# Kernel tuning notes

Hardware: AMD Instinct MI355X
Metric: run time of the kernel (lower is better)

## Reference

```python
import jax, jax.numpy as jnp
import numpy as np

NEG_SLOPE = 0.2  # PyG GATConv default negative_slope


def _gat_layer(x, src, dst, N, W, a_src, a_dst, b):
    """One PyG-style GATConv (eval mode, add_self_loops already applied).
    W: [F_in, H*D], a_src/a_dst: [H, D], b: [H*D]. Returns [N, H*D] (concat)."""
    H, D = a_src.shape
    h = (x @ W).reshape(N, H, D)                      # [N,H,D]
    al_s = (h * a_src).sum(-1)                        # [N,H]
    al_d = (h * a_dst).sum(-1)                        # [N,H]
    e = jax.nn.leaky_relu(al_s[src] + al_d[dst], NEG_SLOPE)   # [E,H]
    # softmax over incoming edges of each destination node
    m = jax.lax.stop_gradient(jax.ops.segment_max(e, dst, num_segments=N))
    ex = jnp.exp(e - m[dst])
    s = jax.ops.segment_sum(ex, dst, num_segments=N)  # [N,H]
    alpha = ex / s[dst]                               # [E,H]
    msg = h[src] * alpha[:, :, None]                  # [E,H,D]
    out = jax.ops.segment_sum(msg, dst, num_segments=N)
    return out.reshape(N, H * D) + b


def setup_inputs() -> dict:
    key = jax.random.key(0)
    ks = jax.random.split(key, 16)
    N, E, F_in, HID, HEADS, C = 50000, 1600000, 128, 8, 8, 16
    x = jax.random.normal(ks[0], (N, F_in), dtype=jnp.float32)
    edge_index = jax.random.randint(ks[1], (2, E), 0, N, dtype=jnp.int64)

    def glorot(k, shape):
        fan = shape[0] + shape[-1]
        return jax.random.uniform(k, shape, jnp.float32, -1.0, 1.0) * np.sqrt(6.0 / fan)

    HD = HID * HEADS  # 64
    return {
        "x": x, "edge_index": edge_index,
        "W1": glorot(ks[2], (F_in, HD)), "a1s": glorot(ks[3], (HEADS, HID)),
        "a1d": glorot(ks[4], (HEADS, HID)), "b1": jnp.zeros((HD,), jnp.float32),
        "W2": glorot(ks[5], (HD, HD)), "a2s": glorot(ks[6], (HEADS, HID)),
        "a2d": glorot(ks[7], (HEADS, HID)), "b2": jnp.zeros((HD,), jnp.float32),
        "W3": glorot(ks[8], (HD, HD)), "a3s": glorot(ks[9], (HEADS, HID)),
        "a3d": glorot(ks[10], (HEADS, HID)), "b3": jnp.zeros((HD,), jnp.float32),
        "W4": glorot(ks[11], (HD, C)), "a4s": glorot(ks[12], (1, C)),
        "a4d": glorot(ks[13], (1, C)), "b4": jnp.zeros((C,), jnp.float32),
    }


def reference(x, edge_index, W1, a1s, a1d, b1, W2, a2s, a2d, b2,
              W3, a3s, a3d, b3, W4, a4s, a4d, b4):
    N = x.shape[0]
    loops = jnp.arange(N, dtype=edge_index.dtype)  # PyG add_self_loops=True
    src = jnp.concatenate([edge_index[0], loops])
    dst = jnp.concatenate([edge_index[1], loops])
    h = jax.nn.relu(_gat_layer(x, src, dst, N, W1, a1s, a1d, b1))
    h = jax.nn.relu(_gat_layer(h, src, dst, N, W2, a2s, a2d, b2))
    h = jax.nn.relu(_gat_layer(h, src, dst, N, W3, a3s, a3d, b3))
    return _gat_layer(h, src, dst, N, W4, a4s, a4d, b4)  # [N, num_classes]
```

## Files before the change

### kernel.cpp

```cpp
#include <hip/hip_runtime.h>
#include <hip/hip_bf16.h>
#include <math.h>

#define NEG_SLOPE 0.2f
#define LOGIT_SHIFT 8.0f

static inline int cdiv(int a, int b) { return (a + b - 1) / b; }

#define BCAP 12288
#define PT_THREADS 512
#define PT_EPT 16
#define PT_CHUNK (PT_THREADS * PT_EPT)

__global__ __launch_bounds__(PT_THREADS)
void partition_kernel(const int* __restrict__ src, const int* __restrict__ dst,
                      unsigned* __restrict__ gcursor, unsigned* __restrict__ slab,
                      int E, int ET, int NBK) {
    __shared__ int hist[256];
    __shared__ int lbase[256];
    __shared__ int lcur[256];
    __shared__ int gbase[256];
    __shared__ unsigned stage[PT_CHUNK];
    __shared__ unsigned char binof[PT_CHUNK];

    int base = blockIdx.x * PT_CHUNK;
    int cnt = min(PT_CHUNK, ET - base);

    unsigned vals[PT_EPT];
    short bins[PT_EPT];

    for (int i = threadIdx.x; i < 256; i += PT_THREADS) hist[i] = 0;
    __syncthreads();

#pragma unroll
    for (int i = 0; i < PT_EPT; ++i) {
        int e = base + threadIdx.x + i * PT_THREADS;
        bins[i] = -1;
        if (e < ET) {
            int s = (e < E) ? src[e] : (e - E);
            int d = (e < E) ? dst[e] : (e - E);
            int b = d >> 8;
            vals[i] = ((unsigned)s << 8) | (unsigned)(d & 255);
            bins[i] = (short)b;
            atomicAdd(&hist[b], 1);
        }
    }
    __syncthreads();
    if (threadIdx.x < 256) lbase[threadIdx.x] = hist[threadIdx.x];
    __syncthreads();
    for (int off = 1; off < 256; off <<= 1) {
        int t = 0;
        if (threadIdx.x < 256 && threadIdx.x >= off) t = lbase[threadIdx.x - off];
        __syncthreads();
        if (threadIdx.x < 256) lbase[threadIdx.x] += t;
        __syncthreads();
    }
    if (threadIdx.x < 256) {
        lbase[threadIdx.x] -= hist[threadIdx.x];
        lcur[threadIdx.x] = lbase[threadIdx.x];
        gbase[threadIdx.x] = ((int)threadIdx.x < NBK && hist[threadIdx.x] > 0)
            ? (int)atomicAdd(&gcursor[threadIdx.x], (unsigned)hist[threadIdx.x]) : 0;
    }
    __syncthreads();
#pragma unroll
    for (int i = 0; i < PT_EPT; ++i) {
        if (bins[i] >= 0) {
            int p = atomicAdd(&lcur[bins[i]], 1);
            stage[p] = vals[i];
            binof[p] = (unsigned char)bins[i];
        }
    }
    __syncthreads();
    for (int j = threadIdx.x; j < cnt; j += PT_THREADS) {
        int b = binof[j];
        int idx = gbase[b] + (j - lbase[b]);
        if (idx < BCAP) slab[(size_t)b * BCAP + idx] = stage[j];
    }
}

__global__ __launch_bounds__(512)
void finalize_kernel(const unsigned* __restrict__ gcursor, unsigned* __restrict__ slab,
                     int* __restrict__ offs, int* __restrict__ deg, int N) {
    __shared__ int lhist[256];
    __shared__ int loff[256];
    __shared__ int lcur[256];
    __shared__ unsigned stage[BCAP];
    int b = blockIdx.x;
    int cnt = min((int)gcursor[b], BCAP);
    int d0 = b << 8;
    int nd = min(256, N - d0);
    size_t sb = (size_t)b * BCAP;

    for (int i = threadIdx.x; i < 256; i += 512) lhist[i] = 0;
    __syncthreads();
    for (int i = threadIdx.x; i < cnt; i += 512)
        atomicAdd(&lhist[slab[sb + i] & 255u], 1);
    __syncthreads();
    if (threadIdx.x < 256) loff[threadIdx.x] = lhist[threadIdx.x];
    __syncthreads();
    for (int off = 1; off < 256; off <<= 1) {
        int t = 0;
        if (threadIdx.x < 256 && threadIdx.x >= off) t = loff[threadIdx.x - off];
        __syncthreads();
        if (threadIdx.x < 256) loff[threadIdx.x] += t;
        __syncthreads();
    }
    if (threadIdx.x < 256) {
        loff[threadIdx.x] -= lhist[threadIdx.x];
        lcur[threadIdx.x] = loff[threadIdx.x];
        if ((int)threadIdx.x < nd) {
            offs[d0 + threadIdx.x] = (int)sb + loff[threadIdx.x];
            deg[d0 + threadIdx.x] = lhist[threadIdx.x];
        }
    }
    __syncthreads();
    for (int i = threadIdx.x; i < cnt; i += 512) {
        unsigned v = slab[sb + i];
        int p = atomicAdd(&lcur[v & 255u], 1);
        stage[p] = v >> 8;
    }
    __syncthreads();
    for (int i = threadIdx.x; i < cnt; i += 512)
        slab[sb + i] = stage[i];
}

template <int CIN, int COUT, int H, bool BF16OUT>
__global__ void gemm_logits_kernel(const float* __restrict__ in, const float* __restrict__ W,
                                   const float* __restrict__ a_s, const float* __restrict__ a_d,
                                   void* __restrict__ outv, float* __restrict__ als,
                                   float* __restrict__ ald, int N) {
    constexpr int D = COUT / H;
    constexpr int TPN = COUT / 4;
    constexpr int NPB = 256 / TPN;
    __shared__ float xs[NPB * CIN];
    __shared__ float lsum[2][NPB][H];
    int n0 = blockIdx.x * NPB;
    for (int i = threadIdx.x * 4; i < NPB * CIN; i += 256 * 4) {
        int n = n0 + i / CIN;
        float4 v = make_float4(0.f, 0.f, 0.f, 0.f);
        if (n < N) v = *(const float4*)&in[(size_t)n0 * CIN + i];
        *(float4*)&xs[i] = v;
    }
    for (int i = threadIdx.x; i < 2 * NPB * H; i += 256) ((float*)lsum)[i] = 0.f;
    __syncthreads();
    int tn = threadIdx.x / TPN;
    int tc = (threadIdx.x % TPN) * 4;
    int n = n0 + tn;
    if (n < N) {
        const float* xr = xs + tn * CIN;
        float4 a = make_float4(0.f, 0.f, 0.f, 0.f);
#pragma unroll 8
        for (int k = 0; k < CIN; ++k) {
            float xv = xr[k];
            float4 wv = *(const float4*)&W[k * COUT + tc];
            a.x = fmaf(xv, wv.x, a.x);
            a.y = fmaf(xv, wv.y, a.y);
            a.z = fmaf(xv, wv.z, a.z);
            a.w = fmaf(xv, wv.w, a.w);
        }
        if (BF16OUT) {
            __hip_bfloat16* ob = (__hip_bfloat16*)outv;
            ushort4 u;
            u.x = __hip_bfloat16_raw(__float2bfloat16(a.x)).x;
            u.y = __hip_bfloat16_raw(__float2bfloat16(a.y)).x;
            u.z = __hip_bfloat16_raw(__float2bfloat16(a.z)).x;
            u.w = __hip_bfloat16_raw(__float2bfloat16(a.w)).x;
            *(ushort4*)&ob[(size_t)n * COUT + tc] = u;
        } else {
            float* of = (float*)outv;
            *(float4*)&of[(size_t)n * COUT + tc] = a;
        }
        int h = tc / D;
        int dd = tc % D;
        const float* asr = a_s + h * D + dd;
        const float* adr = a_d + h * D + dd;
        float p1 = a.x * asr[0] + a.y * asr[1] + a.z * asr[2] + a.w * asr[3];
        float p2 = a.x * adr[0] + a.y * adr[1] + a.z * adr[2] + a.w * adr[3];
        atomicAdd(&lsum[0][tn][h], p1);
        atomicAdd(&lsum[1][tn][h], p2);
    }
    __syncthreads();
    for (int i = threadIdx.x; i < NPB * H; i += 256) {
        int tn2 = i / H, h2 = i % H;
        int n2 = n0 + tn2;
        if (n2 < N) {
            als[n2 * H + h2] = lsum[0][tn2][h2];
            ald[n2 * H + h2] = lsum[1][tn2][h2];
        }
    }
}

__device__ __forceinline__ float lrelu(float x) {
    return (x > 0.f) ? x : NEG_SLOPE * x;
}
__device__ __forceinline__ float edge_w(float logit) {
    return __expf(lrelu(logit) - LOGIT_SHIFT);
}

template <bool RELU>
__global__ void gat_node8_kernel(const __hip_bfloat16* __restrict__ hfeat,
                                 const float* __restrict__ als, const float* __restrict__ ald,
                                 const int* __restrict__ offs, const int* __restrict__ deg,
                                 const int* __restrict__ csr_src,
                                 const float* __restrict__ bias,
                                 float* __restrict__ out, int N) {
    int lane = threadIdx.x & 63;
    int wid = threadIdx.x >> 6;
    int node = blockIdx.x * (blockDim.x >> 6) + wid;
    if (node >= N) return;
    int row = __builtin_amdgcn_readfirstlane(offs[node]);
    int cnt = __builtin_amdgcn_readfirstlane(deg[node]);

    int hl = lane & 7;
    int el = lane >> 3;
    float xd = ald[node * 8 + hl];

    float s0 = 0.f, s1 = 0.f;
    int k = el;
    for (; k + 8 < cnt; k += 16) {
        int snA = csr_src[row + k];
        int snB = csr_src[row + k + 8];
        s0 += edge_w(als[snA * 8 + hl] + xd);
        s1 += edge_w(als[snB * 8 + hl] + xd);
    }
    if (k < cnt) {
        int sn = csr_src[row + k];
        s0 += edge_w(als[sn * 8 + hl] + xd);
    }
    float sl = s0 + s1;
    sl += __shfl_xor(sl, 8);
    sl += __shfl_xor(sl, 16);
    sl += __shfl_xor(sl, 32);

    int c = lane;
    int h2 = lane >> 3;
    float s2 = __shfl(sl, h2);
    float acc = 0.f;
    int kk = el;
    int kc = (kk < cnt) ? kk : (cnt - 1);
    int sn_l = csr_src[row + kc];
    float w_l = (kk < cnt) ? edge_w(als[sn_l * 8 + hl] + xd) : 0.f;
    for (int kb = 0; kb < cnt; kb += 8) {
        int sn_cur = sn_l;
        float w_cur = w_l;
        int kk2 = kb + 8 + el;
        if (kb + 8 < cnt) {
            int kc2 = (kk2 < cnt) ? kk2 : (cnt - 1);
            sn_l = csr_src[row + kc2];
            w_l = (kk2 < cnt) ? edge_w(als[sn_l * 8 + hl] + xd) : 0.f;
        }
#pragma unroll
        for (int e = 0; e < 8; ++e) {
            int srcl = (e << 3) + h2;
            int sn_e = __shfl(sn_cur, srcl);
            float w_e = __shfl(w_cur, srcl);
            float hv = __bfloat162float(hfeat[(size_t)sn_e * 64 + c]);
            acc = fmaf(w_e, hv, acc);
        }
    }
    float v = acc / s2 + bias[c];
    if (RELU) v = fmaxf(v, 0.f);
    out[(size_t)node * 64 + c] = v;
}

__global__ void gat_node16_kernel(const float* __restrict__ hfeat,
                                  const float* __restrict__ als, const float* __restrict__ ald,
                                  const int* __restrict__ offs, const int* __restrict__ deg,
                                  const int* __restrict__ csr_src,
                                  const float* __restrict__ bias,
                                  float* __restrict__ out, int N) {
    int lane = threadIdx.x & 63;
    int wid = threadIdx.x >> 6;
    int node = blockIdx.x * (blockDim.x >> 6) + wid;
    if (node >= N) return;
    int row = __builtin_amdgcn_readfirstlane(offs[node]);
    int cnt = __builtin_amdgcn_readfirstlane(deg[node]);
    float xd = ald[node];

    float s0 = 0.f, s1 = 0.f;
    int k = lane;
    for (; k + 64 < cnt; k += 128) {
        int snA = csr_src[row + k];
        int snB = csr_src[row + k + 64];
        s0 += edge_w(als[snA] + xd);
        s1 += edge_w(als[snB] + xd);
    }
    if (k < cnt) {
        int sn = csr_src[row + k];
        s0 += edge_w(als[sn] + xd);
    }
    float sl = s0 + s1;
#pragma unroll
    for (int off = 1; off < 64; off <<= 1) sl += __shfl_xor(sl, off);

    int c = lane & 15;
    int g = lane >> 4;
    float a0 = 0.f, a1 = 0.f, a2 = 0.f, a3 = 0.f;
    k = g;
    for (; k + 12 < cnt; k += 16) {
        int sn0 = csr_src[row + k];
        int sn1 = csr_src[row + k + 4];
        int sn2 = csr_src[row + k + 8];
        int sn3 = csr_src[row + k + 12];
        float w0 = edge_w(als[sn0] + xd);
        float w1 = edge_w(als[sn1] + xd);
        float w2 = edge_w(als[sn2] + xd);
        float w3 = edge_w(als[sn3] + xd);
        a0 = fmaf(w0, hfeat[(size_t)sn0 * 16 + c], a0);
        a1 = fmaf(w1, hfeat[(size_t)sn1 * 16 + c], a1);
        a2 = fmaf(w2, hfeat[(size_t)sn2 * 16 + c], a2);
        a3 = fmaf(w3, hfeat[(size_t)sn3 * 16 + c], a3);
    }
    for (; k < cnt; k += 4) {
        int sn = csr_src[row + k];
        a0 = fmaf(edge_w(als[sn] + xd), hfeat[(size_t)sn * 16 + c], a0);
    }
    float acc = (a0 + a1) + (a2 + a3);
    acc += __shfl_xor(acc, 16);
    acc += __shfl_xor(acc, 32);
    if (lane < 16) {
        out[(size_t)node * 16 + c] = acc / sl + bias[c];
    }
}


extern "C" void kernel_launch(void* const* d_in, const int* in_sizes, int n_in,
                              void* d_out, int out_size, void* d_ws, size_t ws_size,
                              hipStream_t stream) {
    const float* x   = (const float*)d_in[0];
    const int*   ei  = (const int*)d_in[1];
    const float* W1  = (const float*)d_in[2];
    const float* a1s = (const float*)d_in[3];
    const float* a1d = (const float*)d_in[4];
    const float* b1  = (const float*)d_in[5];
    const float* W2  = (const float*)d_in[6];
    const float* a2s = (const float*)d_in[7];
    const float* a2d = (const float*)d_in[8];
    const float* b2  = (const float*)d_in[9];
    const float* W3  = (const float*)d_in[10];
    const float* a3s = (const float*)d_in[11];
    const float* a3d = (const float*)d_in[12];
    const float* b3  = (const float*)d_in[13];
    const float* W4  = (const float*)d_in[14];
    const float* a4s = (const float*)d_in[15];
    const float* a4d = (const float*)d_in[16];
    const float* b4  = (const float*)d_in[17];

    const int N = in_sizes[0] / 128;
    const int E = in_sizes[1] / 2;
    const int ET = E + N;
    const int* src = ei;
    const int* dst = ei + E;
    const int NBK = (N + 255) >> 8;

    float* hb    = (float*)d_ws;
    float* bufA  = hb + (size_t)N * 64;
    float* als   = bufA + (size_t)N * 64;
    float* ald   = als + (size_t)N * 8;
    int* offs    = (int*)(ald + (size_t)N * 8);
    int* deg     = offs + N;
    unsigned* gcursor = (unsigned*)(deg + N);
    unsigned* slab = gcursor + 256;
    float* out = (float*)d_out;

    __hip_bfloat16* hb16 = (__hip_bfloat16*)hb;

    const int TB = 256;
    const int NODE_BLOCKS = cdiv(N, 4);

    hipMemsetAsync(gcursor, 0, 256 * 4, stream);
    partition_kernel<<<cdiv(ET, PT_CHUNK), PT_THREADS, 0, stream>>>(src, dst, gcursor, slab, E, ET, NBK);
    finalize_kernel<<<NBK, 512, 0, stream>>>(gcursor, slab, offs, deg, N);
    const int* csr_src = (const int*)slab;

    gemm_logits_kernel<128, 64, 8, true><<<cdiv(N, 16), TB, 0, stream>>>(x, W1, a1s, a1d, hb16, als, ald, N);
    gat_node8_kernel<true><<<NODE_BLOCKS, TB, 0, stream>>>(hb16, als, ald, offs, deg, csr_src, b1, bufA, N);

    gemm_logits_kernel<64, 64, 8, true><<<cdiv(N, 16), TB, 0, stream>>>(bufA, W2, a2s, a2d, hb16, als, ald, N);
    gat_node8_kernel<true><<<NODE_BLOCKS, TB, 0, stream>>>(hb16, als, ald, offs, deg, csr_src, b2, bufA, N);

    gemm_logits_kernel<64, 64, 8, true><<<cdiv(N, 16), TB, 0, stream>>>(bufA, W3, a3s, a3d, hb16, als, ald, N);
    gat_node8_kernel<true><<<NODE_BLOCKS, TB, 0, stream>>>(hb16, als, ald, offs, deg, csr_src, b3, bufA, N);

    gemm_logits_kernel<64, 16, 1, false><<<cdiv(N, 64), TB, 0, stream>>>(bufA, W4, a4s, a4d, hb, als, ald, N);
    gat_node16_kernel<<<NODE_BLOCKS, TB, 0, stream>>>(hb, als, ald, offs, deg, csr_src, b4, out, N);
}
```

Measured before the change: 491.2 us.

## Fuse softmax denominator into single-pass aggregation with vectorized per-edge feature loads

Both GAT node kernels drop the separate pass that computed the softmax denominator. Each lane now owns one edge and one head/column chunk, loads 8 bf16 (or 4 fp32) features as a single vector, and accumulates the weighted sum and the denominator together. Partial results are then reduced with cross-lane shuffles. This removes the duplicate csr_src/als gathers and the per-edge shuffles of the old code, at the cost of more registers and a longer butterfly reduction at the end.

```diff
diff --git a/kernel.cpp b/kernel.cpp
--- a/kernel.cpp
+++ b/kernel.cpp
@@ -211,56 +211,64 @@
     int row = __builtin_amdgcn_readfirstlane(offs[node]);
     int cnt = __builtin_amdgcn_readfirstlane(deg[node]);
 
-    int hl = lane & 7;
     int el = lane >> 3;
-    float xd = ald[node * 8 + hl];
-
-    float s0 = 0.f, s1 = 0.f;
-    int k = el;
-    for (; k + 8 < cnt; k += 16) {
-        int snA = csr_src[row + k];
-        int snB = csr_src[row + k + 8];
-        s0 += edge_w(als[snA * 8 + hl] + xd);
-        s1 += edge_w(als[snB * 8 + hl] + xd);
-    }
-    if (k < cnt) {
-        int sn = csr_src[row + k];
-        s0 += edge_w(als[sn * 8 + hl] + xd);
-    }
-    float sl = s0 + s1;
-    sl += __shfl_xor(sl, 8);
-    sl += __shfl_xor(sl, 16);
-    sl += __shfl_xor(sl, 32);
-
-    int c = lane;
-    int h2 = lane >> 3;
-    float s2 = __shfl(sl, h2);
-    float acc = 0.f;
+    int cb = lane & 7;
+    float xd = ald[node * 8 + cb];
+
+    float s = 0.f;
+    float acc[8];
+#pragma unroll
+    for (int j = 0; j < 8; ++j) acc[j] = 0.f;
+
     int kk = el;
     int kc = (kk < cnt) ? kk : (cnt - 1);
-    int sn_l = csr_src[row + kc];
-    float w_l = (kk < cnt) ? edge_w(als[sn_l * 8 + hl] + xd) : 0.f;
+    int sn_c = csr_src[row + kc];
+    float al_c = als[sn_c * 8 + cb];
+    uint4 hv_c = *(const uint4*)(hfeat + (size_t)sn_c * 64 + cb * 8);
+    bool va_c = (kk < cnt);
+
     for (int kb = 0; kb < cnt; kb += 8) {
-        int sn_cur = sn_l;
-        float w_cur = w_l;
-        int kk2 = kb + 8 + el;
+        int sn_n = sn_c; float al_n = 0.f; uint4 hv_n = hv_c; bool va_n = false;
         if (kb + 8 < cnt) {
+            int kk2 = kb + 8 + el;
             int kc2 = (kk2 < cnt) ? kk2 : (cnt - 1);
-            sn_l = csr_src[row + kc2];
-            w_l = (kk2 < cnt) ? edge_w(als[sn_l * 8 + hl] + xd) : 0.f;
-        }
-#pragma unroll
-        for (int e = 0; e < 8; ++e) {
-            int srcl = (e << 3) + h2;
-            int sn_e = __shfl(sn_cur, srcl);
-            float w_e = __shfl(w_cur, srcl);
-            float hv = __bfloat162float(hfeat[(size_t)sn_e * 64 + c]);
-            acc = fmaf(w_e, hv, acc);
-        }
-    }
-    float v = acc / s2 + bias[c];
-    if (RELU) v = fmaxf(v, 0.f);
-    out[(size_t)node * 64 + c] = v;
+            sn_n = csr_src[row + kc2];
+            al_n = als[sn_n * 8 + cb];
+            hv_n = *(const uint4*)(hfeat + (size_t)sn_n * 64 + cb * 8);
+            va_n = (kk2 < cnt);
+        }
+        float w = va_c ? edge_w(al_c + xd) : 0.f;
+        s += w;
+        const ushort* hu = (const ushort*)&hv_c;
+#pragma unroll
+        for (int j = 0; j < 8; ++j) {
+            float f = __uint_as_float(((unsigned)hu[j]) << 16);
+            acc[j] = fmaf(w, f, acc[j]);
+        }
+        sn_c = sn_n; al_c = al_n; hv_c = hv_n; va_c = va_n;
+    }
+
+    s += __shfl_xor(s, 8); s += __shfl_xor(s, 16); s += __shfl_xor(s, 32);
+#pragma unroll
+    for (int j = 0; j < 8; ++j) {
+        acc[j] += __shfl_xor(acc[j], 8);
+        acc[j] += __shfl_xor(acc[j], 16);
+        acc[j] += __shfl_xor(acc[j], 32);
+    }
+
+    if (el == 0) {
+        float inv = 1.f / s;
+        float o[8];
+#pragma unroll
+        for (int j = 0; j < 8; ++j) {
+            float v = acc[j] * inv + bias[cb * 8 + j];
+            if (RELU) v = fmaxf(v, 0.f);
+            o[j] = v;
+        }
+        float4* op = (float4*)(out + (size_t)node * 64 + cb * 8);
+        op[0] = make_float4(o[0], o[1], o[2], o[3]);
+        op[1] = make_float4(o[4], o[5], o[6], o[7]);
+    }
 }
 
 __global__ void gat_node16_kernel(const float* __restrict__ hfeat,
@@ -275,51 +283,57 @@
     if (node >= N) return;
     int row = __builtin_amdgcn_readfirstlane(offs[node]);
     int cnt = __builtin_amdgcn_readfirstlane(deg[node]);
+
+    int el = lane >> 2;
+    int cq = lane & 3;
     float xd = ald[node];
 
-    float s0 = 0.f, s1 = 0.f;
-    int k = lane;
-    for (; k + 64 < cnt; k += 128) {
-        int snA = csr_src[row + k];
-        int snB = csr_src[row + k + 64];
-        s0 += edge_w(als[snA] + xd);
-        s1 += edge_w(als[snB] + xd);
-    }
-    if (k < cnt) {
-        int sn = csr_src[row + k];
-        s0 += edge_w(als[sn] + xd);
-    }
-    float sl = s0 + s1;
-#pragma unroll
-    for (int off = 1; off < 64; off <<= 1) sl += __shfl_xor(sl, off);
-
-    int c = lane & 15;
-    int g = lane >> 4;
-    float a0 = 0.f, a1 = 0.f, a2 = 0.f, a3 = 0.f;
-    k = g;
-    for (; k + 12 < cnt; k += 16) {
-        int sn0 = csr_src[row + k];
-        int sn1 = csr_src[row + k + 4];
-        int sn2 = csr_src[row + k + 8];
-        int sn3 = csr_src[row + k + 12];
-        float w0 = edge_w(als[sn0] + xd);
-        float w1 = edge_w(als[sn1] + xd);
-        float w2 = edge_w(als[sn2] + xd);
-        float w3 = edge_w(als[sn3] + xd);
-        a0 = fmaf(w0, hfeat[(size_t)sn0 * 16 + c], a0);
-        a1 = fmaf(w1, hfeat[(size_t)sn1 * 16 + c], a1);
-        a2 = fmaf(w2, hfeat[(size_t)sn2 * 16 + c], a2);
-        a3 = fmaf(w3, hfeat[(size_t)sn3 * 16 + c], a3);
-    }
-    for (; k < cnt; k += 4) {
-        int sn = csr_src[row + k];
-        a0 = fmaf(edge_w(als[sn] + xd), hfeat[(size_t)sn * 16 + c], a0);
-    }
-    float acc = (a0 + a1) + (a2 + a3);
-    acc += __shfl_xor(acc, 16);
-    acc += __shfl_xor(acc, 32);
-    if (lane < 16) {
-        out[(size_t)node * 16 + c] = acc / sl + bias[c];
+    float s = 0.f;
+    float4 acc = make_float4(0.f, 0.f, 0.f, 0.f);
+
+    int kk = el;
+    int kc = (kk < cnt) ? kk : (cnt - 1);
+    int sn_c = csr_src[row + kc];
+    float al_c = als[sn_c];
+    float4 hv_c = *(const float4*)(hfeat + (size_t)sn_c * 16 + cq * 4);
+    bool va_c = (kk < cnt);
+
+    for (int kb = 0; kb < cnt; kb += 16) {
+        int sn_n = sn_c; float al_n = 0.f; float4 hv_n = hv_c; bool va_n = false;
+        if (kb + 16 < cnt) {
+            int kk2 = kb + 16 + el;
+            int kc2 = (kk2 < cnt) ? kk2 : (cnt - 1);
+            sn_n = csr_src[row + kc2];
+            al_n = als[sn_n];
+            hv_n = *(const float4*)(hfeat + (size_t)sn_n * 16 + cq * 4);
+            va_n = (kk2 < cnt);
+        }
+        float w = va_c ? edge_w(al_c + xd) : 0.f;
+        s += w;
+        acc.x = fmaf(w, hv_c.x, acc.x);
+        acc.y = fmaf(w, hv_c.y, acc.y);
+        acc.z = fmaf(w, hv_c.z, acc.z);
+        acc.w = fmaf(w, hv_c.w, acc.w);
+        sn_c = sn_n; al_c = al_n; hv_c = hv_n; va_c = va_n;
+    }
+
+    s += __shfl_xor(s, 4); s += __shfl_xor(s, 8); s += __shfl_xor(s, 16); s += __shfl_xor(s, 32);
+#pragma unroll
+    for (int r = 4; r < 64; r <<= 1) {
+        acc.x += __shfl_xor(acc.x, r);
+        acc.y += __shfl_xor(acc.y, r);
+        acc.z += __shfl_xor(acc.z, r);
+        acc.w += __shfl_xor(acc.w, r);
+    }
+
+    if (el == 0) {
+        float inv = 1.f / s;
+        float4 o;
+        o.x = acc.x * inv + bias[cq * 4 + 0];
+        o.y = acc.y * inv + bias[cq * 4 + 1];
+        o.z = acc.z * inv + bias[cq * 4 + 2];
+        o.w = acc.w * inv + bias[cq * 4 + 3];
+        *(float4*)(out + (size_t)node * 16 + cq * 4) = o;
     }
 }
 
```

Result: faster. 411.5 us (-16.2%).
